# Optimization experiments

Hardware: AMD Instinct MI355X
Metric: run time of the kernel (lower is better)

The kernel has to match this reference:

```python
import jax, jax.numpy as jnp
import numpy as np

N = 200000
C = 256
RATIO = 0.5
K = max(int(N * RATIO), 1)  # 100000 clusters kept


def setup_inputs() -> dict:
    key = jax.random.key(0)
    k1, k2, k3, k4 = jax.random.split(key, 4)
    x = jax.random.normal(k1, (N, C), dtype=jnp.float32)
    edge_index = jax.random.randint(k2, (2, N), 0, N, dtype=jnp.int32)  # E == N (source requires it)
    batch = jnp.zeros((N,), dtype=jnp.int32)
    # nn.Linear(C, 1): weight [1, C] -> flattened to [C]; bias [1] -> scalar
    w = jax.random.normal(k3, (C,), dtype=jnp.float32) * (1.0 / np.sqrt(C))
    b = jax.random.normal(k4, (1,), dtype=jnp.float32) * 0.01
    return {"x": x, "edge_index": edge_index, "batch": batch, "w": w, "b": b}


def reference(x, edge_index, batch, w, b):
    # scores = tanh(Linear(x)) over nodes: [N]
    scores = jnp.tanh(x @ w + b[0])
    # top-k node selection (torch uses sorted=False; ordering within topk is unspecified,
    # we use lax.top_k's sorted-descending order deterministically)
    _, perm = jax.lax.top_k(scores, K)  # [K] int32
    x_pool = x[perm]                    # [K, C]
    # mask is True for NON-selected nodes (as in the source)
    mask = jnp.ones((N,), dtype=bool).at[perm].set(False)
    # exactly N-K True entries (perm indices are distinct) -> static shape
    keep = jnp.nonzero(mask, size=N - K)[0]  # positions into edge rows (E == N)
    # relabel map: old node id -> new pooled id (0 for dropped nodes, as in source)
    new_mask = jnp.zeros((N,), dtype=jnp.int32).at[perm].set(jnp.arange(K, dtype=jnp.int32))
    ei = new_mask[edge_index[0][keep]]
    ej = new_mask[edge_index[1][keep]]
    edge_index_pool = jnp.stack([ei, ej], axis=0)  # [2, N-K]
    batch_pool = batch[perm]
    return (x_pool, edge_index_pool, perm, batch_pool, scores[perm])
```

## Files before the change

kernel.cpp:

```cpp
#include <hip/hip_runtime.h>

typedef unsigned long long u64;
typedef unsigned int u32;

#define NN 200000
#define CC 256
#define KK 100000
#define TILE 2048
#define NB ((NN + TILE - 1) / TILE)

#define OFF_X     0
#define OFF_E0    25600000
#define OFF_E1    25700000
#define OFF_PERM  25800000
#define OFF_BATCH 25900000
#define OFF_SC    26000000

__device__ __forceinline__ u32 key_of_f32(float s) {
    u32 b = __float_as_uint(s);
    u32 u = b ^ ((b & 0x80000000u) ? 0xFFFFFFFFu : 0x80000000u);
    return ~u;
}

__device__ __forceinline__ float xla_tanhf(float x) {
    const float kMax = (float)7.90531110763549805;
    float xc = fminf(fmaxf(x, -kMax), kMax);
    float x2 = __fmul_rn(xc, xc);
    float p = (float)-2.76076847742355e-16;
    p = __fadd_rn(__fmul_rn(p, x2), (float)2.00018790482477e-13);
    p = __fadd_rn(__fmul_rn(p, x2), (float)-8.60467152213735e-11);
    p = __fadd_rn(__fmul_rn(p, x2), (float)5.12229709037114e-08);
    p = __fadd_rn(__fmul_rn(p, x2), (float)1.48572235717979e-05);
    p = __fadd_rn(__fmul_rn(p, x2), (float)6.37261928875436e-04);
    p = __fadd_rn(__fmul_rn(p, x2), (float)4.89352455891786e-03);
    float num = __fmul_rn(xc, p);
    float q = (float)1.19825839466702e-06;
    q = __fadd_rn(__fmul_rn(q, x2), (float)1.18534705686654e-04);
    q = __fadd_rn(__fmul_rn(q, x2), (float)2.26843463243900e-03);
    q = __fadd_rn(__fmul_rn(q, x2), (float)4.89352518554385e-03);
    float t = __fdiv_rn(num, q);
    return (fabsf(x) < 0.0004f) ? x : t;
}

__global__ void score_kernel(const float* __restrict__ x, const float* __restrict__ w,
                             const float* __restrict__ b, u32* __restrict__ keys,
                             u32* __restrict__ vals, float* __restrict__ scoreF,
                             int* __restrict__ mark) {
    int i = (int)(blockIdx.x * blockDim.x + threadIdx.x);
    if (i >= NN) return;
    const float4* row = (const float4*)(x + (size_t)i * CC);
    const float4* wv  = (const float4*)w;
    float c0 = 0.f, c1 = 0.f, c2 = 0.f, c3 = 0.f;
    float c4 = 0.f, c5 = 0.f, c6 = 0.f, c7 = 0.f;
#pragma unroll 8
    for (int t = 0; t < 32; ++t) {
        float4 a0 = row[2 * t], a1 = row[2 * t + 1];
        float4 w0 = wv[2 * t],  w1 = wv[2 * t + 1];
        c0 = __builtin_fmaf(a0.x, w0.x, c0);
        c1 = __builtin_fmaf(a0.y, w0.y, c1);
        c2 = __builtin_fmaf(a0.z, w0.z, c2);
        c3 = __builtin_fmaf(a0.w, w0.w, c3);
        c4 = __builtin_fmaf(a1.x, w1.x, c4);
        c5 = __builtin_fmaf(a1.y, w1.y, c5);
        c6 = __builtin_fmaf(a1.z, w1.z, c6);
        c7 = __builtin_fmaf(a1.w, w1.w, c7);
    }
    float d0 = __fadd_rn(c0, c1);
    float d1 = __fadd_rn(c2, c3);
    float d2 = __fadd_rn(c4, c5);
    float d3 = __fadd_rn(c6, c7);
    float e0 = __fadd_rn(d0, d1);
    float e1 = __fadd_rn(d2, d3);
    float dot = __fadd_rn(e0, e1);
    float z = __fadd_rn(dot, b[0]);
    float s = xla_tanhf(z);
    keys[i]   = key_of_f32(s);
    vals[i]   = (u32)i;
    scoreF[i] = s;
    mark[i]   = 0;
}


__global__ void radix_count(const u32* __restrict__ keys, int shift,
                            u32* __restrict__ counts , int n) {
    __shared__ u32 hist[256];
    hist[threadIdx.x] = 0;
    __syncthreads();
    int wv = threadIdx.x >> 6, lane = threadIdx.x & 63;
    int base = blockIdx.x * TILE + wv * 512;
#pragma unroll
    for (int e = 0; e < 8; ++e) {
        int i = base + e * 64 + lane;
        if (i < n) {
            u32 d = (keys[i] >> shift) & 255u;
            atomicAdd(&hist[d], 1u);
        }
    }
    __syncthreads();
    counts[blockIdx.x * 256 + threadIdx.x] = hist[threadIdx.x];
}

__global__ void radix_scatter(const u32* __restrict__ keysIn, const u32* __restrict__ valsIn,
                              u32* __restrict__ keysOut, u32* __restrict__ valsOut,
                              int shift, const u32* __restrict__ counts, int n) {
    __shared__ u32 waveCnt[4][256];
    __shared__ u32 tot[256];
    __shared__ u32 scanbuf[256];
    int tid = threadIdx.x;
    int wv = tid >> 6, lane = tid & 63;

    u32 myprefix = 0, total = 0;
    int myb = blockIdx.x;
#pragma unroll 7
    for (int bb = 0; bb < NB; ++bb) {
        u32 c = counts[bb * 256 + tid];
        if (bb < myb) myprefix += c;
        total += c;
    }
    tot[tid] = total;
    scanbuf[tid] = total;
    __syncthreads();
#pragma unroll
    for (int off = 1; off < 256; off <<= 1) {
        u32 v = (tid >= off) ? scanbuf[tid - off] : 0u;
        __syncthreads();
        scanbuf[tid] += v;
        __syncthreads();
    }
    u32 globalBase = (scanbuf[tid] - tot[tid]) + myprefix;

#pragma unroll
    for (int w = 0; w < 4; ++w) waveCnt[w][tid] = 0;
    __syncthreads();

    int base = blockIdx.x * TILE + wv * 512;
    u32 k[8];
    u64 peers[8];
    u32 dg[8];
    int valid[8];
#pragma unroll
    for (int e = 0; e < 8; ++e) {
        int i = base + e * 64 + lane;
        valid[e] = (i < n);
        k[e] = valid[e] ? keysIn[i] : 0u;
        dg[e] = (k[e] >> shift) & 255u;
    }
#pragma unroll
    for (int e = 0; e < 8; ++e) {
        u64 vm = __ballot(valid[e]);
        u64 mask = vm;
#pragma unroll
        for (int bit = 0; bit < 8; ++bit) {
            u64 bal = __ballot(valid[e] && ((dg[e] >> bit) & 1u));
            mask &= ((dg[e] >> bit) & 1u) ? bal : ~bal;
        }
        peers[e] = mask;
        if (valid[e]) {
            u64 lower = mask & ((1ull << lane) - 1ull);
            if (lower == 0ull)
                waveCnt[wv][dg[e]] += (u32)__popcll(mask);
        }
    }
    __syncthreads();
    {
        u32 r = globalBase;
#pragma unroll
        for (int w = 0; w < 4; ++w) { u32 c = waveCnt[w][tid]; waveCnt[w][tid] = r; r += c; }
    }
    __syncthreads();
#pragma unroll
    for (int e = 0; e < 8; ++e) {
        if (valid[e]) {
            u64 mask = peers[e];
            u64 lower = mask & ((1ull << lane) - 1ull);
            u32 rk = (u32)__popcll(lower);
            u32 pos = waveCnt[wv][dg[e]] + rk;
            keysOut[pos] = k[e];
            valsOut[pos] = valsIn[base + e * 64 + lane];
            if (lower == 0ull) waveCnt[wv][dg[e]] += (u32)__popcll(mask);
        }
    }
}


__global__ void gather_sel(const float* __restrict__ x, const u32* __restrict__ vals,
                           const float* __restrict__ scoreF, const int* __restrict__ batch,
                           float* __restrict__ out, int* __restrict__ mark) {
    int kI = (int)((blockIdx.x * blockDim.x + threadIdx.x) >> 6);
    int lane = threadIdx.x & 63;
    if (kI >= KK) return;
    u32 idx = vals[kI];
    const float4* src = (const float4*)(x + (size_t)idx * CC);
    float4* dst = (float4*)(out + OFF_X + (size_t)kI * CC);
    dst[lane] = src[lane];
    if (lane == 0) {
        out[OFF_PERM + kI]  = (float)idx;
        out[OFF_SC + kI]    = scoreF[idx];
        out[OFF_BATCH + kI] = (float)batch[idx];
        mark[idx] = kI + 1;
    }
}

__global__ void keep_count(const int* __restrict__ mark, u32* __restrict__ blockCnt) {
    __shared__ u32 wsum[4];
    int wv = threadIdx.x >> 6, lane = threadIdx.x & 63;
    if (threadIdx.x < 4) wsum[threadIdx.x] = 0;
    __syncthreads();
    int base = blockIdx.x * TILE + wv * 512;
    u32 cnt = 0;
#pragma unroll
    for (int e = 0; e < 8; ++e) {
        int i = base + e * 64 + lane;
        if (i < NN && mark[i] == 0) cnt++;
    }
#pragma unroll
    for (int off = 32; off > 0; off >>= 1) cnt += __shfl_xor(cnt, off);
    if (lane == 0) wsum[wv] = cnt;
    __syncthreads();
    if (threadIdx.x == 0) blockCnt[blockIdx.x] = wsum[0] + wsum[1] + wsum[2] + wsum[3];
}

__global__ void edge_scatter(const int* __restrict__ mark, const int* __restrict__ e0,
                             const int* __restrict__ e1, const u32* __restrict__ blockCnt,
                             float* __restrict__ out) {
    __shared__ u32 wbase[4];
    __shared__ u32 bOff;
    int tid = threadIdx.x, wv = tid >> 6, lane = tid & 63;
    if (tid == 0) {
        u32 r = 0;
        for (int bb = 0; bb < blockIdx.x; ++bb) r += blockCnt[bb];
        bOff = r;
    }
    int base = blockIdx.x * TILE + wv * 512;
    bool flag[8];
    u32 cnt = 0;
#pragma unroll
    for (int e = 0; e < 8; ++e) {
        int i = base + e * 64 + lane;
        flag[e] = (i < NN) && (mark[i] == 0);
        if (flag[e]) cnt++;
    }
    u32 wc = cnt;
#pragma unroll
    for (int off = 32; off > 0; off >>= 1) wc += __shfl_xor(wc, off);
    if (lane == 0) wbase[wv] = wc;
    __syncthreads();
    if (tid == 0) {
        u32 r = bOff;
#pragma unroll
        for (int w = 0; w < 4; ++w) { u32 c = wbase[w]; wbase[w] = r; r += c; }
    }
    __syncthreads();
    u32 run = wbase[wv];
#pragma unroll
    for (int e = 0; e < 8; ++e) {
        u64 bal = __ballot(flag[e]);
        if (flag[e]) {
            u32 pos = run + (u32)__popcll(bal & ((1ull << lane) - 1ull));
            int i = base + e * 64 + lane;
            int a = mark[e0[i]] - 1; if (a < 0) a = 0;
            int c = mark[e1[i]] - 1; if (c < 0) c = 0;
            out[OFF_E0 + pos] = (float)a;
            out[OFF_E1 + pos] = (float)c;
        }
        run += (u32)__popcll(bal);
    }
}

extern "C" void kernel_launch(void* const* d_in, const int* in_sizes, int n_in,
                              void* d_out, int out_size, void* d_ws, size_t ws_size,
                              hipStream_t stream) {
    (void)in_sizes; (void)n_in; (void)out_size; (void)ws_size;
    const float* x     = (const float*)d_in[0];
    const int*   ei    = (const int*)d_in[1];
    const int*   batch = (const int*)d_in[2];
    const float* w     = (const float*)d_in[3];
    const float* b     = (const float*)d_in[4];
    float* out = (float*)d_out;

    char* p = (char*)d_ws;
    u32* keys0 = (u32*)p;            p += (size_t)NN * 4;
    u32* keys1 = (u32*)p;            p += (size_t)NN * 4;
    u32* vals0 = (u32*)p;            p += (size_t)NN * 4;
    u32* vals1 = (u32*)p;            p += (size_t)NN * 4;
    float* scoreF = (float*)p;       p += (size_t)NN * 4;
    int* mark = (int*)p;             p += (size_t)NN * 4;
    u32* counts = (u32*)p;           p += (size_t)NB * 256 * 4;
    u32* blockCnt = (u32*)p;         p += (size_t)NB * 4;

    score_kernel<<<(NN + 255) / 256, 256, 0, stream>>>(x, w, b, keys0, vals0, scoreF, mark);

    for (int pass = 0; pass < 4; ++pass) {
        const u32* ki = (pass & 1) ? keys1 : keys0;
        const u32* vi = (pass & 1) ? vals1 : vals0;
        u32* ko = (pass & 1) ? keys0 : keys1;
        u32* vo = (pass & 1) ? vals0 : vals1;
        radix_count<<<NB, 256, 0, stream>>>(ki, pass * 8, counts, NN);
        radix_scatter<<<NB, 256, 0, stream>>>(ki, vi, ko, vo, pass * 8, counts, NN);
    }

    gather_sel<<<KK * 64 / 256, 256, 0, stream>>>(x, vals0, scoreF, batch, out, mark);
    keep_count<<<NB, 256, 0, stream>>>(mark, blockCnt);
    edge_scatter<<<NB, 256, 0, stream>>>(mark, ei, ei + NN, blockCnt, out);
}
```

Before: 181.6 us.

## Use 11-bit radix digits to cut sort passes from four to three

Changes the LSD radix sort from four 8-bit passes to three 11-bit passes (2048 buckets), which removes one count/scatter kernel pair. The per-block histograms and the bucket scan grow eightfold, and the scan now runs over 2048 entries with more barrier steps. The result lands in keys1/vals1, so the mark buffer reuses keys0 and is cleared with a memset instead of inside the score kernel. The risks are heavier prefix reads of the counts array in every scatter block and more LDS use per block, which may lower occupancy.

```diff
diff --git a/kernel.cpp b/kernel.cpp
--- a/kernel.cpp
+++ b/kernel.cpp
@@ -8,6 +8,8 @@
 #define KK 100000
 #define TILE 2048
 #define NB ((NN + TILE - 1) / TILE)
+#define DIG 2048
+#define DPT (DIG / 256)
 
 #define OFF_X     0
 #define OFF_E0    25600000
@@ -44,8 +46,7 @@
 
 __global__ void score_kernel(const float* __restrict__ x, const float* __restrict__ w,
                              const float* __restrict__ b, u32* __restrict__ keys,
-                             u32* __restrict__ vals, float* __restrict__ scoreF,
-                             int* __restrict__ mark) {
+                             u32* __restrict__ vals, float* __restrict__ scoreF) {
     int i = (int)(blockIdx.x * blockDim.x + threadIdx.x);
     if (i >= NN) return;
     const float4* row = (const float4*)(x + (size_t)i * CC);
@@ -77,60 +78,78 @@
     keys[i]   = key_of_f32(s);
     vals[i]   = (u32)i;
     scoreF[i] = s;
-    mark[i]   = 0;
 }
 
 
 __global__ void radix_count(const u32* __restrict__ keys, int shift,
                             u32* __restrict__ counts , int n) {
-    __shared__ u32 hist[256];
-    hist[threadIdx.x] = 0;
-    __syncthreads();
-    int wv = threadIdx.x >> 6, lane = threadIdx.x & 63;
+    __shared__ u32 hist[DIG];
+    int tid = threadIdx.x;
+#pragma unroll
+    for (int j = 0; j < DPT; ++j) hist[tid + 256 * j] = 0;
+    __syncthreads();
+    int wv = tid >> 6, lane = tid & 63;
     int base = blockIdx.x * TILE + wv * 512;
 #pragma unroll
     for (int e = 0; e < 8; ++e) {
         int i = base + e * 64 + lane;
         if (i < n) {
-            u32 d = (keys[i] >> shift) & 255u;
+            u32 d = (keys[i] >> shift) & (DIG - 1u);
             atomicAdd(&hist[d], 1u);
         }
     }
     __syncthreads();
-    counts[blockIdx.x * 256 + threadIdx.x] = hist[threadIdx.x];
+#pragma unroll
+    for (int j = 0; j < DPT; ++j)
+        counts[blockIdx.x * DIG + tid + 256 * j] = hist[tid + 256 * j];
 }
 
 __global__ void radix_scatter(const u32* __restrict__ keysIn, const u32* __restrict__ valsIn,
                               u32* __restrict__ keysOut, u32* __restrict__ valsOut,
                               int shift, const u32* __restrict__ counts, int n) {
-    __shared__ u32 waveCnt[4][256];
-    __shared__ u32 tot[256];
-    __shared__ u32 scanbuf[256];
+    __shared__ u32 waveCnt[4][DIG];
+    __shared__ u32 scanbuf[DIG];
+    __shared__ u32 gb[DIG];
     int tid = threadIdx.x;
     int wv = tid >> 6, lane = tid & 63;
-
-    u32 myprefix = 0, total = 0;
     int myb = blockIdx.x;
-#pragma unroll 7
+
+    u32 totR[DPT], preR[DPT];
+#pragma unroll
+    for (int j = 0; j < DPT; ++j) { totR[j] = 0; preR[j] = 0; }
     for (int bb = 0; bb < NB; ++bb) {
-        u32 c = counts[bb * 256 + tid];
-        if (bb < myb) myprefix += c;
-        total += c;
-    }
-    tot[tid] = total;
-    scanbuf[tid] = total;
-    __syncthreads();
-#pragma unroll
-    for (int off = 1; off < 256; off <<= 1) {
-        u32 v = (tid >= off) ? scanbuf[tid - off] : 0u;
+#pragma unroll
+        for (int j = 0; j < DPT; ++j) {
+            u32 c = counts[bb * DIG + tid + 256 * j];
+            if (bb < myb) preR[j] += c;
+            totR[j] += c;
+        }
+    }
+#pragma unroll
+    for (int j = 0; j < DPT; ++j) scanbuf[tid + 256 * j] = totR[j];
+    __syncthreads();
+    for (int off = 1; off < DIG; off <<= 1) {
+        u32 v[DPT];
+#pragma unroll
+        for (int j = 0; j < DPT; ++j) {
+            int d = tid + 256 * j;
+            v[j] = (d >= off) ? scanbuf[d - off] : 0u;
+        }
         __syncthreads();
-        scanbuf[tid] += v;
+#pragma unroll
+        for (int j = 0; j < DPT; ++j) scanbuf[tid + 256 * j] += v[j];
         __syncthreads();
     }
-    u32 globalBase = (scanbuf[tid] - tot[tid]) + myprefix;
-
-#pragma unroll
-    for (int w = 0; w < 4; ++w) waveCnt[w][tid] = 0;
+#pragma unroll
+    for (int j = 0; j < DPT; ++j) {
+        int d = tid + 256 * j;
+        gb[d] = (scanbuf[d] - totR[j]) + preR[j];
+    }
+#pragma unroll
+    for (int j = 0; j < DPT; ++j) {
+#pragma unroll
+        for (int w = 0; w < 4; ++w) waveCnt[w][tid + 256 * j] = 0;
+    }
     __syncthreads();
 
     int base = blockIdx.x * TILE + wv * 512;
@@ -143,14 +162,14 @@
         int i = base + e * 64 + lane;
         valid[e] = (i < n);
         k[e] = valid[e] ? keysIn[i] : 0u;
-        dg[e] = (k[e] >> shift) & 255u;
+        dg[e] = (k[e] >> shift) & (DIG - 1u);
     }
 #pragma unroll
     for (int e = 0; e < 8; ++e) {
         u64 vm = __ballot(valid[e]);
         u64 mask = vm;
 #pragma unroll
-        for (int bit = 0; bit < 8; ++bit) {
+        for (int bit = 0; bit < 11; ++bit) {
             u64 bal = __ballot(valid[e] && ((dg[e] >> bit) & 1u));
             mask &= ((dg[e] >> bit) & 1u) ? bal : ~bal;
         }
@@ -162,10 +181,12 @@
         }
     }
     __syncthreads();
-    {
-        u32 r = globalBase;
-#pragma unroll
-        for (int w = 0; w < 4; ++w) { u32 c = waveCnt[w][tid]; waveCnt[w][tid] = r; r += c; }
+#pragma unroll
+    for (int j = 0; j < DPT; ++j) {
+        int d = tid + 256 * j;
+        u32 r = gb[d];
+#pragma unroll
+        for (int w = 0; w < 4; ++w) { u32 c = waveCnt[w][d]; waveCnt[w][d] = r; r += c; }
     }
     __syncthreads();
 #pragma unroll
@@ -284,22 +305,24 @@
     u32* vals0 = (u32*)p;            p += (size_t)NN * 4;
     u32* vals1 = (u32*)p;            p += (size_t)NN * 4;
     float* scoreF = (float*)p;       p += (size_t)NN * 4;
-    int* mark = (int*)p;             p += (size_t)NN * 4;
-    u32* counts = (u32*)p;           p += (size_t)NB * 256 * 4;
+    u32* counts = (u32*)p;           p += (size_t)NB * DIG * 4;
     u32* blockCnt = (u32*)p;         p += (size_t)NB * 4;
-
-    score_kernel<<<(NN + 255) / 256, 256, 0, stream>>>(x, w, b, keys0, vals0, scoreF, mark);
-
-    for (int pass = 0; pass < 4; ++pass) {
+    int* mark = (int*)keys0;
+
+    score_kernel<<<(NN + 255) / 256, 256, 0, stream>>>(x, w, b, keys0, vals0, scoreF);
+
+    for (int pass = 0; pass < 3; ++pass) {
         const u32* ki = (pass & 1) ? keys1 : keys0;
         const u32* vi = (pass & 1) ? vals1 : vals0;
         u32* ko = (pass & 1) ? keys0 : keys1;
         u32* vo = (pass & 1) ? vals0 : vals1;
-        radix_count<<<NB, 256, 0, stream>>>(ki, pass * 8, counts, NN);
-        radix_scatter<<<NB, 256, 0, stream>>>(ki, vi, ko, vo, pass * 8, counts, NN);
-    }
-
-    gather_sel<<<KK * 64 / 256, 256, 0, stream>>>(x, vals0, scoreF, batch, out, mark);
+        radix_count<<<NB, 256, 0, stream>>>(ki, pass * 11, counts, NN);
+        radix_scatter<<<NB, 256, 0, stream>>>(ki, vi, ko, vo, pass * 11, counts, NN);
+    }
+
+    hipMemsetAsync(mark, 0, (size_t)NN * sizeof(int), stream);
+
+    gather_sel<<<KK * 64 / 256, 256, 0, stream>>>(x, vals1, scoreF, batch, out, mark);
     keep_count<<<NB, 256, 0, stream>>>(mark, blockCnt);
     edge_scatter<<<NB, 256, 0, stream>>>(mark, ei, ei + NN, blockCnt, out);
 }
```

Measured after the change: 262.9 us. +44.8%, slower.

## Fuse radix count/scatter and edge count/scatter via software grid barriers

Applied to the files above, without the earlier changes.

Merges each radix-sort histogram kernel with its scatter kernel into one launch, separated by an atomic-counter grid barrier. The edge keep-count and edge scatter are fused the same way, and the block offset becomes a wave reduction instead of a serial loop. The last pass no longer writes keys. This removes several kernel launches and a second read of the keys per pass. It relies on all 98 blocks being co-resident for the spin barrier; if they are not, it deadlocks.

```diff
diff --git a/kernel.cpp b/kernel.cpp
--- a/kernel.cpp
+++ b/kernel.cpp
@@ -45,8 +45,9 @@
 __global__ void score_kernel(const float* __restrict__ x, const float* __restrict__ w,
                              const float* __restrict__ b, u32* __restrict__ keys,
                              u32* __restrict__ vals, float* __restrict__ scoreF,
-                             int* __restrict__ mark) {
+                             int* __restrict__ mark, u32* __restrict__ gsync) {
     int i = (int)(blockIdx.x * blockDim.x + threadIdx.x);
+    if (blockIdx.x == 0 && threadIdx.x < 8) gsync[threadIdx.x] = 0;
     if (i >= NN) return;
     const float4* row = (const float4*)(x + (size_t)i * CC);
     const float4* wv  = (const float4*)w;
@@ -80,37 +81,64 @@
     mark[i]   = 0;
 }
 
-
-__global__ void radix_count(const u32* __restrict__ keys, int shift,
-                            u32* __restrict__ counts , int n) {
-    __shared__ u32 hist[256];
-    hist[threadIdx.x] = 0;
-    __syncthreads();
-    int wv = threadIdx.x >> 6, lane = threadIdx.x & 63;
-    int base = blockIdx.x * TILE + wv * 512;
+__device__ __forceinline__ void grid_barrier(u32* gsync, int tid) {
+    __syncthreads();
+    if (tid == 0) {
+        __threadfence();
+        atomicAdd(gsync, 1u);
+        while (__hip_atomic_load(gsync, __ATOMIC_RELAXED, __HIP_MEMORY_SCOPE_AGENT) < (u32)NB)
+            __builtin_amdgcn_s_sleep(1);
+        __threadfence();
+    }
+    __syncthreads();
+}
+
+__global__ void radix_pass(const u32* __restrict__ keysIn, const u32* __restrict__ valsIn,
+                           u32* __restrict__ keysOut, u32* __restrict__ valsOut,
+                           int shift, u32* __restrict__ counts, u32* __restrict__ gsync,
+                           int writeKeys, int n) {
+    __shared__ u32 waveCnt[4][256];
+    __shared__ u32 scanbuf[256];
+    __shared__ u32 tot[256];
+    int tid = threadIdx.x, wv = tid >> 6, lane = tid & 63, myb = blockIdx.x;
+#pragma unroll
+    for (int w = 0; w < 4; ++w) waveCnt[w][tid] = 0;
+    __syncthreads();
+
+    int base = myb * TILE + wv * 512;
+    u32 k[8];
+    u64 peers[8];
+    u32 dg[8];
+    int valid[8];
 #pragma unroll
     for (int e = 0; e < 8; ++e) {
         int i = base + e * 64 + lane;
-        if (i < n) {
-            u32 d = (keys[i] >> shift) & 255u;
-            atomicAdd(&hist[d], 1u);
-        }
-    }
-    __syncthreads();
-    counts[blockIdx.x * 256 + threadIdx.x] = hist[threadIdx.x];
-}
-
-__global__ void radix_scatter(const u32* __restrict__ keysIn, const u32* __restrict__ valsIn,
-                              u32* __restrict__ keysOut, u32* __restrict__ valsOut,
-                              int shift, const u32* __restrict__ counts, int n) {
-    __shared__ u32 waveCnt[4][256];
-    __shared__ u32 tot[256];
-    __shared__ u32 scanbuf[256];
-    int tid = threadIdx.x;
-    int wv = tid >> 6, lane = tid & 63;
+        valid[e] = (i < n);
+        k[e] = valid[e] ? keysIn[i] : 0u;
+        dg[e] = (k[e] >> shift) & 255u;
+    }
+#pragma unroll
+    for (int e = 0; e < 8; ++e) {
+        u64 mask = __ballot(valid[e]);
+#pragma unroll
+        for (int bit = 0; bit < 8; ++bit) {
+            u64 bal = __ballot(valid[e] && ((dg[e] >> bit) & 1u));
+            mask &= ((dg[e] >> bit) & 1u) ? bal : ~bal;
+        }
+        peers[e] = mask;
+        if (valid[e]) {
+            u64 lower = mask & ((1ull << lane) - 1ull);
+            if (lower == 0ull)
+                waveCnt[wv][dg[e]] += (u32)__popcll(mask);
+        }
+    }
+    __syncthreads();
+    counts[myb * 256 + tid] =
+        waveCnt[0][tid] + waveCnt[1][tid] + waveCnt[2][tid] + waveCnt[3][tid];
+
+    grid_barrier(gsync, tid);
 
     u32 myprefix = 0, total = 0;
-    int myb = blockIdx.x;
 #pragma unroll 7
     for (int bb = 0; bb < NB; ++bb) {
         u32 c = counts[bb * 256 + tid];
@@ -128,40 +156,6 @@
         __syncthreads();
     }
     u32 globalBase = (scanbuf[tid] - tot[tid]) + myprefix;
-
-#pragma unroll
-    for (int w = 0; w < 4; ++w) waveCnt[w][tid] = 0;
-    __syncthreads();
-
-    int base = blockIdx.x * TILE + wv * 512;
-    u32 k[8];
-    u64 peers[8];
-    u32 dg[8];
-    int valid[8];
-#pragma unroll
-    for (int e = 0; e < 8; ++e) {
-        int i = base + e * 64 + lane;
-        valid[e] = (i < n);
-        k[e] = valid[e] ? keysIn[i] : 0u;
-        dg[e] = (k[e] >> shift) & 255u;
-    }
-#pragma unroll
-    for (int e = 0; e < 8; ++e) {
-        u64 vm = __ballot(valid[e]);
-        u64 mask = vm;
-#pragma unroll
-        for (int bit = 0; bit < 8; ++bit) {
-            u64 bal = __ballot(valid[e] && ((dg[e] >> bit) & 1u));
-            mask &= ((dg[e] >> bit) & 1u) ? bal : ~bal;
-        }
-        peers[e] = mask;
-        if (valid[e]) {
-            u64 lower = mask & ((1ull << lane) - 1ull);
-            if (lower == 0ull)
-                waveCnt[wv][dg[e]] += (u32)__popcll(mask);
-        }
-    }
-    __syncthreads();
     {
         u32 r = globalBase;
 #pragma unroll
@@ -175,7 +169,7 @@
             u64 lower = mask & ((1ull << lane) - 1ull);
             u32 rk = (u32)__popcll(lower);
             u32 pos = waveCnt[wv][dg[e]] + rk;
-            keysOut[pos] = k[e];
+            if (writeKeys) keysOut[pos] = k[e];
             valsOut[pos] = valsIn[base + e * 64 + lane];
             if (lower == 0ull) waveCnt[wv][dg[e]] += (u32)__popcll(mask);
         }
@@ -201,37 +195,13 @@
     }
 }
 
-__global__ void keep_count(const int* __restrict__ mark, u32* __restrict__ blockCnt) {
-    __shared__ u32 wsum[4];
-    int wv = threadIdx.x >> 6, lane = threadIdx.x & 63;
-    if (threadIdx.x < 4) wsum[threadIdx.x] = 0;
-    __syncthreads();
-    int base = blockIdx.x * TILE + wv * 512;
-    u32 cnt = 0;
-#pragma unroll
-    for (int e = 0; e < 8; ++e) {
-        int i = base + e * 64 + lane;
-        if (i < NN && mark[i] == 0) cnt++;
-    }
-#pragma unroll
-    for (int off = 32; off > 0; off >>= 1) cnt += __shfl_xor(cnt, off);
-    if (lane == 0) wsum[wv] = cnt;
-    __syncthreads();
-    if (threadIdx.x == 0) blockCnt[blockIdx.x] = wsum[0] + wsum[1] + wsum[2] + wsum[3];
-}
-
-__global__ void edge_scatter(const int* __restrict__ mark, const int* __restrict__ e0,
-                             const int* __restrict__ e1, const u32* __restrict__ blockCnt,
-                             float* __restrict__ out) {
+__global__ void edge_pass(const int* __restrict__ mark, const int* __restrict__ e0,
+                          const int* __restrict__ e1, u32* __restrict__ blockCnt,
+                          u32* __restrict__ gsync, float* __restrict__ out) {
     __shared__ u32 wbase[4];
-    __shared__ u32 bOff;
-    int tid = threadIdx.x, wv = tid >> 6, lane = tid & 63;
-    if (tid == 0) {
-        u32 r = 0;
-        for (int bb = 0; bb < blockIdx.x; ++bb) r += blockCnt[bb];
-        bOff = r;
-    }
-    int base = blockIdx.x * TILE + wv * 512;
+    __shared__ u32 wsum2[4];
+    int tid = threadIdx.x, wv = tid >> 6, lane = tid & 63, myb = blockIdx.x;
+    int base = myb * TILE + wv * 512;
     bool flag[8];
     u32 cnt = 0;
 #pragma unroll
@@ -245,6 +215,17 @@
     for (int off = 32; off > 0; off >>= 1) wc += __shfl_xor(wc, off);
     if (lane == 0) wbase[wv] = wc;
     __syncthreads();
+    if (tid == 0) blockCnt[myb] = wbase[0] + wbase[1] + wbase[2] + wbase[3];
+
+    grid_barrier(gsync, tid);
+
+    u32 v = (tid < myb) ? blockCnt[tid] : 0u;
+#pragma unroll
+    for (int off = 32; off > 0; off >>= 1) v += __shfl_xor(v, off);
+    if (lane == 0) wsum2[wv] = v;
+    __syncthreads();
+    u32 bOff = wsum2[0] + wsum2[1] + wsum2[2] + wsum2[3];
+
     if (tid == 0) {
         u32 r = bOff;
 #pragma unroll
@@ -287,19 +268,16 @@
     int* mark = (int*)p;             p += (size_t)NN * 4;
     u32* counts = (u32*)p;           p += (size_t)NB * 256 * 4;
     u32* blockCnt = (u32*)p;         p += (size_t)NB * 4;
-
-    score_kernel<<<(NN + 255) / 256, 256, 0, stream>>>(x, w, b, keys0, vals0, scoreF, mark);
-
-    for (int pass = 0; pass < 4; ++pass) {
-        const u32* ki = (pass & 1) ? keys1 : keys0;
-        const u32* vi = (pass & 1) ? vals1 : vals0;
-        u32* ko = (pass & 1) ? keys0 : keys1;
-        u32* vo = (pass & 1) ? vals0 : vals1;
-        radix_count<<<NB, 256, 0, stream>>>(ki, pass * 8, counts, NN);
-        radix_scatter<<<NB, 256, 0, stream>>>(ki, vi, ko, vo, pass * 8, counts, NN);
-    }
+    u32* gsync = (u32*)p;            p += 8 * 4;
+
+    score_kernel<<<(NN + 255) / 256, 256, 0, stream>>>(x, w, b, keys0, vals0, scoreF,
+                                                       mark, gsync);
+
+    radix_pass<<<NB, 256, 0, stream>>>(keys0, vals0, keys1, vals1,  0, counts, gsync + 0, 1, NN);
+    radix_pass<<<NB, 256, 0, stream>>>(keys1, vals1, keys0, vals0,  8, counts, gsync + 1, 1, NN);
+    radix_pass<<<NB, 256, 0, stream>>>(keys0, vals0, keys1, vals1, 16, counts, gsync + 2, 1, NN);
+    radix_pass<<<NB, 256, 0, stream>>>(keys1, vals1, keys0, vals0, 24, counts, gsync + 3, 0, NN);
 
     gather_sel<<<KK * 64 / 256, 256, 0, stream>>>(x, vals0, scoreF, batch, out, mark);
-    keep_count<<<NB, 256, 0, stream>>>(mark, blockCnt);
-    edge_scatter<<<NB, 256, 0, stream>>>(mark, ei, ei + NN, blockCnt, out);
-}
+    edge_pass<<<NB, 256, 0, stream>>>(mark, ei, ei + NN, blockCnt, gsync + 4, out);
+}
```

After: 231.0 us. 27.2% more time.

## Fuse first radix histogram into score kernel and drop keep_count pass

Applied to the files above, without the earlier changes.

The score kernel now builds the digit-0 histogram in shared memory, so the first radix_count launch disappears. radix_scatter accepts a variable number of count blocks and, on the last pass, zeroes the mark array, which reuses the counts0 buffer. The keep_count kernel is removed: edge_scatter works out each tile's offset by counting selected indices below the tile start across the whole vals array. The cost is a scan of all K selected indices per edge_scatter block and a longer prefix loop in the first scatter pass (782 count blocks).

```diff
diff --git a/kernel.cpp b/kernel.cpp
--- a/kernel.cpp
+++ b/kernel.cpp
@@ -8,6 +8,7 @@
 #define KK 100000
 #define TILE 2048
 #define NB ((NN + TILE - 1) / TILE)
+#define SB ((NN + 255) / 256)
 
 #define OFF_X     0
 #define OFF_E0    25600000
@@ -45,41 +46,48 @@
 __global__ void score_kernel(const float* __restrict__ x, const float* __restrict__ w,
                              const float* __restrict__ b, u32* __restrict__ keys,
                              u32* __restrict__ vals, float* __restrict__ scoreF,
-                             int* __restrict__ mark) {
-    int i = (int)(blockIdx.x * blockDim.x + threadIdx.x);
-    if (i >= NN) return;
-    const float4* row = (const float4*)(x + (size_t)i * CC);
-    const float4* wv  = (const float4*)w;
-    float c0 = 0.f, c1 = 0.f, c2 = 0.f, c3 = 0.f;
-    float c4 = 0.f, c5 = 0.f, c6 = 0.f, c7 = 0.f;
+                             u32* __restrict__ counts0) {
+    __shared__ u32 hist[256];
+    int tid = threadIdx.x;
+    hist[tid] = 0;
+    __syncthreads();
+    int i = (int)(blockIdx.x * blockDim.x + tid);
+    if (i < NN) {
+        const float4* row = (const float4*)(x + (size_t)i * CC);
+        const float4* wv  = (const float4*)w;
+        float c0 = 0.f, c1 = 0.f, c2 = 0.f, c3 = 0.f;
+        float c4 = 0.f, c5 = 0.f, c6 = 0.f, c7 = 0.f;
 #pragma unroll 8
-    for (int t = 0; t < 32; ++t) {
-        float4 a0 = row[2 * t], a1 = row[2 * t + 1];
-        float4 w0 = wv[2 * t],  w1 = wv[2 * t + 1];
-        c0 = __builtin_fmaf(a0.x, w0.x, c0);
-        c1 = __builtin_fmaf(a0.y, w0.y, c1);
-        c2 = __builtin_fmaf(a0.z, w0.z, c2);
-        c3 = __builtin_fmaf(a0.w, w0.w, c3);
-        c4 = __builtin_fmaf(a1.x, w1.x, c4);
-        c5 = __builtin_fmaf(a1.y, w1.y, c5);
-        c6 = __builtin_fmaf(a1.z, w1.z, c6);
-        c7 = __builtin_fmaf(a1.w, w1.w, c7);
-    }
-    float d0 = __fadd_rn(c0, c1);
-    float d1 = __fadd_rn(c2, c3);
-    float d2 = __fadd_rn(c4, c5);
-    float d3 = __fadd_rn(c6, c7);
-    float e0 = __fadd_rn(d0, d1);
-    float e1 = __fadd_rn(d2, d3);
-    float dot = __fadd_rn(e0, e1);
-    float z = __fadd_rn(dot, b[0]);
-    float s = xla_tanhf(z);
-    keys[i]   = key_of_f32(s);
-    vals[i]   = (u32)i;
-    scoreF[i] = s;
-    mark[i]   = 0;
-}
-
+        for (int t = 0; t < 32; ++t) {
+            float4 a0 = row[2 * t], a1 = row[2 * t + 1];
+            float4 w0 = wv[2 * t],  w1 = wv[2 * t + 1];
+            c0 = __builtin_fmaf(a0.x, w0.x, c0);
+            c1 = __builtin_fmaf(a0.y, w0.y, c1);
+            c2 = __builtin_fmaf(a0.z, w0.z, c2);
+            c3 = __builtin_fmaf(a0.w, w0.w, c3);
+            c4 = __builtin_fmaf(a1.x, w1.x, c4);
+            c5 = __builtin_fmaf(a1.y, w1.y, c5);
+            c6 = __builtin_fmaf(a1.z, w1.z, c6);
+            c7 = __builtin_fmaf(a1.w, w1.w, c7);
+        }
+        float d0 = __fadd_rn(c0, c1);
+        float d1 = __fadd_rn(c2, c3);
+        float d2 = __fadd_rn(c4, c5);
+        float d3 = __fadd_rn(c6, c7);
+        float e0 = __fadd_rn(d0, d1);
+        float e1 = __fadd_rn(d2, d3);
+        float dot = __fadd_rn(e0, e1);
+        float z = __fadd_rn(dot, b[0]);
+        float s = xla_tanhf(z);
+        u32 key = key_of_f32(s);
+        keys[i]   = key;
+        vals[i]   = (u32)i;
+        scoreF[i] = s;
+        atomicAdd(&hist[key & 255u], 1u);
+    }
+    __syncthreads();
+    counts0[blockIdx.x * 256 + tid] = hist[tid];
+}
 
 __global__ void radix_count(const u32* __restrict__ keys, int shift,
                             u32* __restrict__ counts , int n) {
@@ -102,23 +110,24 @@
 
 __global__ void radix_scatter(const u32* __restrict__ keysIn, const u32* __restrict__ valsIn,
                               u32* __restrict__ keysOut, u32* __restrict__ valsOut,
-                              int shift, const u32* __restrict__ counts, int n) {
+                              int shift, const u32* __restrict__ counts,
+                              int cntBlks, int cbPerTile, int* __restrict__ mark, int n) {
     __shared__ u32 waveCnt[4][256];
+    __shared__ u32 scanbuf[256];
     __shared__ u32 tot[256];
-    __shared__ u32 scanbuf[256];
-    int tid = threadIdx.x;
-    int wv = tid >> 6, lane = tid & 63;
+    int tid = threadIdx.x, wv = tid >> 6, lane = tid & 63, myb = blockIdx.x;
 
     u32 myprefix = 0, total = 0;
-    int myb = blockIdx.x;
-#pragma unroll 7
-    for (int bb = 0; bb < NB; ++bb) {
-        u32 c = counts[bb * 256 + tid];
-        if (bb < myb) myprefix += c;
+    int cbLim = myb * cbPerTile;
+    for (int cb = 0; cb < cntBlks; ++cb) {
+        u32 c = counts[cb * 256 + tid];
+        if (cb < cbLim) myprefix += c;
         total += c;
     }
     tot[tid] = total;
     scanbuf[tid] = total;
+#pragma unroll
+    for (int w = 0; w < 4; ++w) waveCnt[w][tid] = 0;
     __syncthreads();
 #pragma unroll
     for (int off = 1; off < 256; off <<= 1) {
@@ -129,11 +138,7 @@
     }
     u32 globalBase = (scanbuf[tid] - tot[tid]) + myprefix;
 
-#pragma unroll
-    for (int w = 0; w < 4; ++w) waveCnt[w][tid] = 0;
-    __syncthreads();
-
-    int base = blockIdx.x * TILE + wv * 512;
+    int base = myb * TILE + wv * 512;
     u32 k[8];
     u64 peers[8];
     u32 dg[8];
@@ -144,11 +149,11 @@
         valid[e] = (i < n);
         k[e] = valid[e] ? keysIn[i] : 0u;
         dg[e] = (k[e] >> shift) & 255u;
-    }
-#pragma unroll
-    for (int e = 0; e < 8; ++e) {
-        u64 vm = __ballot(valid[e]);
-        u64 mask = vm;
+        if (mark != nullptr && valid[e]) mark[i] = 0;
+    }
+#pragma unroll
+    for (int e = 0; e < 8; ++e) {
+        u64 mask = __ballot(valid[e]);
 #pragma unroll
         for (int bit = 0; bit < 8; ++bit) {
             u64 bal = __ballot(valid[e] && ((dg[e] >> bit) & 1u));
@@ -201,37 +206,21 @@
     }
 }
 
-__global__ void keep_count(const int* __restrict__ mark, u32* __restrict__ blockCnt) {
-    __shared__ u32 wsum[4];
-    int wv = threadIdx.x >> 6, lane = threadIdx.x & 63;
-    if (threadIdx.x < 4) wsum[threadIdx.x] = 0;
-    __syncthreads();
-    int base = blockIdx.x * TILE + wv * 512;
-    u32 cnt = 0;
-#pragma unroll
-    for (int e = 0; e < 8; ++e) {
-        int i = base + e * 64 + lane;
-        if (i < NN && mark[i] == 0) cnt++;
-    }
-#pragma unroll
-    for (int off = 32; off > 0; off >>= 1) cnt += __shfl_xor(cnt, off);
-    if (lane == 0) wsum[wv] = cnt;
-    __syncthreads();
-    if (threadIdx.x == 0) blockCnt[blockIdx.x] = wsum[0] + wsum[1] + wsum[2] + wsum[3];
-}
-
 __global__ void edge_scatter(const int* __restrict__ mark, const int* __restrict__ e0,
-                             const int* __restrict__ e1, const u32* __restrict__ blockCnt,
+                             const int* __restrict__ e1, const u32* __restrict__ vals,
                              float* __restrict__ out) {
     __shared__ u32 wbase[4];
-    __shared__ u32 bOff;
-    int tid = threadIdx.x, wv = tid >> 6, lane = tid & 63;
-    if (tid == 0) {
-        u32 r = 0;
-        for (int bb = 0; bb < blockIdx.x; ++bb) r += blockCnt[bb];
-        bOff = r;
-    }
-    int base = blockIdx.x * TILE + wv * 512;
+    __shared__ u32 wsum2[4];
+    int tid = threadIdx.x, wv = tid >> 6, lane = tid & 63, myb = blockIdx.x;
+    int base = myb * TILE + wv * 512;
+
+    u32 thr = (u32)(myb * TILE);
+    u32 selB = 0;
+    for (int j = tid; j < KK; j += 256) selB += (vals[j] < thr) ? 1u : 0u;
+#pragma unroll
+    for (int off = 32; off > 0; off >>= 1) selB += __shfl_xor(selB, off);
+    if (lane == 0) wsum2[wv] = selB;
+
     bool flag[8];
     u32 cnt = 0;
 #pragma unroll
@@ -245,6 +234,7 @@
     for (int off = 32; off > 0; off >>= 1) wc += __shfl_xor(wc, off);
     if (lane == 0) wbase[wv] = wc;
     __syncthreads();
+    u32 bOff = thr - (wsum2[0] + wsum2[1] + wsum2[2] + wsum2[3]);
     if (tid == 0) {
         u32 r = bOff;
 #pragma unroll
@@ -284,22 +274,24 @@
     u32* vals0 = (u32*)p;            p += (size_t)NN * 4;
     u32* vals1 = (u32*)p;            p += (size_t)NN * 4;
     float* scoreF = (float*)p;       p += (size_t)NN * 4;
-    int* mark = (int*)p;             p += (size_t)NN * 4;
-    u32* counts = (u32*)p;           p += (size_t)NB * 256 * 4;
-    u32* blockCnt = (u32*)p;         p += (size_t)NB * 4;
-
-    score_kernel<<<(NN + 255) / 256, 256, 0, stream>>>(x, w, b, keys0, vals0, scoreF, mark);
-
-    for (int pass = 0; pass < 4; ++pass) {
-        const u32* ki = (pass & 1) ? keys1 : keys0;
-        const u32* vi = (pass & 1) ? vals1 : vals0;
-        u32* ko = (pass & 1) ? keys0 : keys1;
-        u32* vo = (pass & 1) ? vals0 : vals1;
-        radix_count<<<NB, 256, 0, stream>>>(ki, pass * 8, counts, NN);
-        radix_scatter<<<NB, 256, 0, stream>>>(ki, vi, ko, vo, pass * 8, counts, NN);
-    }
+    u32* counts0 = (u32*)p;          p += (size_t)SB * 256 * 4;
+    u32* cs = (u32*)p;               p += (size_t)NB * 256 * 4;
+    int* mark = (int*)counts0;
+
+    score_kernel<<<SB, 256, 0, stream>>>(x, w, b, keys0, vals0, scoreF, counts0);
+
+    radix_scatter<<<NB, 256, 0, stream>>>(keys0, vals0, keys1, vals1,  0, counts0,
+                                          SB, 8, nullptr, NN);
+    radix_count<<<NB, 256, 0, stream>>>(keys1, 8, cs, NN);
+    radix_scatter<<<NB, 256, 0, stream>>>(keys1, vals1, keys0, vals0,  8, cs,
+                                          NB, 1, nullptr, NN);
+    radix_count<<<NB, 256, 0, stream>>>(keys0, 16, cs, NN);
+    radix_scatter<<<NB, 256, 0, stream>>>(keys0, vals0, keys1, vals1, 16, cs,
+                                          NB, 1, nullptr, NN);
+    radix_count<<<NB, 256, 0, stream>>>(keys1, 24, cs, NN);
+    radix_scatter<<<NB, 256, 0, stream>>>(keys1, vals1, keys0, vals0, 24, cs,
+                                          NB, 1, mark, NN);
 
     gather_sel<<<KK * 64 / 256, 256, 0, stream>>>(x, vals0, scoreF, batch, out, mark);
-    keep_count<<<NB, 256, 0, stream>>>(mark, blockCnt);
-    edge_scatter<<<NB, 256, 0, stream>>>(mark, ei, ei + NN, blockCnt, out);
-}
+    edge_scatter<<<NB, 256, 0, stream>>>(mark, ei, ei + NN, vals0, out);
+}
```

Result: slower. 353.5 us (+94.7%).
